# Performance work log

Hardware: AMD Instinct MI355X
Metric: run time of the kernel (lower is better)

## Reference

```python
import jax, jax.numpy as jnp
import numpy as np

N = 50000   # nodes
E = 800000  # edges (avg degree 16)
D = 128     # hidden_channels
L = 4       # num_layers
ALPHA = 0.1


def setup_inputs() -> dict:
    key = jax.random.key(0)
    ks = jax.random.split(key, 6)
    x = jax.random.normal(ks[0], (N, D), dtype=jnp.float32)
    w = jax.random.uniform(ks[1], (E,), dtype=jnp.float32)
    src = jax.random.randint(ks[2], (E,), 0, N)
    dst = jax.random.randint(ks[3], (E,), 0, N)
    # stacked per-layer Linear params
    W = jax.random.normal(ks[4], (L, D, D), dtype=jnp.float32) / np.float32(np.sqrt(D))
    b = jax.random.normal(ks[5], (L, D), dtype=jnp.float32) * 0.01
    # GPR coefficients: alpha*(1-alpha)^k, last = (1-alpha)^L
    temp_np = ALPHA * (1 - ALPHA) ** np.arange(L + 1)
    temp_np[-1] = (1 - ALPHA) ** L
    temp = jnp.asarray(temp_np, dtype=jnp.float32)
    return {"x": x, "w": w, "src": src, "dst": dst, "W": W, "b": b, "temp": temp}


def reference(x, w, src, dst, W, b, temp):
    # eval mode: dropout / dropout_adj are no-ops; edge_attn=False
    hidden = x * temp[0]
    for i in range(L):
        h = x @ W[i] + b[i]                 # [N, D] linear
        msg = h[src] * w[:, None]           # gather + edge-weight, [E, D]
        x = jax.ops.segment_sum(msg, dst, num_segments=N)  # scatter-sum
        x = jax.nn.relu(x)
        hidden = hidden + x * temp[i + 1]
    return hidden
```

## Files before the change

kernel.cpp:

```cpp
#include <hip/hip_runtime.h>
#include <hip/hip_fp16.h>

#define N_NODES 50000
#define N_EDGES 800000
#define DIM 128
#define LAYERS 4
#define SLOT 48
#define EPB 8

typedef __attribute__((ext_vector_type(8))) _Float16 half8;
typedef __attribute__((ext_vector_type(4))) float float4v;

__device__ __forceinline__ int pack_edge(int s, float w) {
    return (int)(((unsigned)__half_as_ushort(__float2half(w)) << 16) | (unsigned)(s & 0xFFFF));
}

__global__ __launch_bounds__(256) void init_kernel(const float4* __restrict__ x,
                                                   __half* __restrict__ xh, int n4) {
    int i = blockIdx.x * 256 + threadIdx.x;
    if (i >= n4) return;
    float4 v = x[i];
    union { __half2 hh[2]; float2 f2; } u;
    u.hh[0] = __floats2half2_rn(v.x, v.y);
    u.hh[1] = __floats2half2_rn(v.z, v.w);
    *(float2*)(xh + (size_t)i * 4) = u.f2;
}

__global__ __launch_bounds__(256) void bucket_kernel(const int* __restrict__ src,
                                                     const int* __restrict__ dst,
                                                     const float* __restrict__ w,
                                                     int* __restrict__ cnt,
                                                     int* __restrict__ edge_buf) {
    int g     = blockIdx.x & 7;
    int chunk = blockIdx.x >> 3;
    int base  = (chunk * 256 + threadIdx.x) * EPB;
    #pragma unroll
    for (int j = 0; j < EPB; j += 4) {
        int e = base + j;
        if (e >= N_EDGES) break;
        int4 d4 = *(const int4*)(dst + e);
        if ((d4.x & 7) == g) {
            int pos = atomicAdd(&cnt[d4.x], 1);
            edge_buf[(size_t)d4.x * SLOT + pos] = pack_edge(src[e + 0], w[e + 0]);
        }
        if ((d4.y & 7) == g) {
            int pos = atomicAdd(&cnt[d4.y], 1);
            edge_buf[(size_t)d4.y * SLOT + pos] = pack_edge(src[e + 1], w[e + 1]);
        }
        if ((d4.z & 7) == g) {
            int pos = atomicAdd(&cnt[d4.z], 1);
            edge_buf[(size_t)d4.z * SLOT + pos] = pack_edge(src[e + 2], w[e + 2]);
        }
        if ((d4.w & 7) == g) {
            int pos = atomicAdd(&cnt[d4.w], 1);
            edge_buf[(size_t)d4.w * SLOT + pos] = pack_edge(src[e + 3], w[e + 3]);
        }
    }
}

__global__ __launch_bounds__(256) void wt_prep_kernel(const float* __restrict__ W,
                                                      __half* __restrict__ Wt) {
    int i = blockIdx.x * 256 + threadIdx.x;
    if (i >= LAYERS * DIM * DIM) return;
    int l   = i >> 14;
    int rem = i & 16383;
    int k = rem >> 7;
    int n = rem & 127;
    Wt[(size_t)l * DIM * DIM + n * DIM + k] = __float2half(W[(size_t)l * DIM * DIM + k * DIM + n]);
}

__device__ __forceinline__ void batch8(const half8* __restrict__ h8,
                                       int m, int base, int cnt_r, int r, int c,
                                       float* accf, float& wsum) {
    half8 v[8]; float wv[8];
    #pragma unroll
    for (int u = 0; u < 8; ++u) {
        int jj = base + u;
        int p  = __shfl(m, (r << 4) | (jj & 15), 64);
        bool live = (jj < cnt_r);
        wv[u] = live
                  ? __half2float(__ushort_as_half((unsigned short)((unsigned)p >> 16)))
                  : 0.f;
        half8 vv = (half8)(0.f);
        if (live) vv = h8[(size_t)(p & 0xFFFF) * 16 + c];
        v[u] = vv;
    }
    #pragma unroll
    for (int u = 0; u < 8; ++u) {
        wsum += wv[u];
        #pragma unroll
        for (int t = 0; t < 8; ++t)
            accf[t] += wv[u] * (float)v[u][t];
    }
}

#define AP 136
template <bool FINAL>
__global__ __launch_bounds__(256) void layer_kernel(const half8* __restrict__ xin8,
                                                    const int* __restrict__ cnt_arr,
                                                    const int* __restrict__ edge_buf,
                                                    const __half* __restrict__ Wt,
                                                    const float* __restrict__ bl,
                                                    __half* __restrict__ xout_h,
                                                    float* __restrict__ hidden,
                                                    const float* __restrict__ temp,
                                                    const float* __restrict__ xf,
                                                    const half8* __restrict__ x1h,
                                                    const half8* __restrict__ x2h) {
    __shared__ __half Ah[16][AP];
    __shared__ float winS[16];
    int tid  = threadIdx.x;
    int wave = tid >> 6;
    int lane = tid & 63;
    int r = lane >> 4;
    int c = lane & 15;
    int node0  = blockIdx.x * 16 + wave * 4;
    int node_r = node0 + r;

    size_t mb = (size_t)node_r * SLOT;
    int m0 = edge_buf[mb + c];
    int m1 = edge_buf[mb + 16 + c];
    int m2 = edge_buf[mb + 32 + c];
    int4 c4 = *(const int4*)(cnt_arr + node0);

    int cnt_r = (r == 0) ? c4.x : (r == 1) ? c4.y : (r == 2) ? c4.z : c4.w;
    int maxc  = max(max(c4.x, c4.y), max(c4.z, c4.w));

    float accf[8];
    #pragma unroll
    for (int t = 0; t < 8; ++t) accf[t] = 0.f;
    float wsum = 0.f;

    batch8(xin8, m0, 0, cnt_r, r, c, accf, wsum);
    batch8(xin8, m0, 8, cnt_r, r, c, accf, wsum);
    if (maxc > 16) {
        batch8(xin8, m1, 16, cnt_r, r, c, accf, wsum);
        batch8(xin8, m1, 24, cnt_r, r, c, accf, wsum);
    }
    if (maxc > 32) {
        batch8(xin8, m2, 32, cnt_r, r, c, accf, wsum);
        batch8(xin8, m2, 40, cnt_r, r, c, accf, wsum);
    }

    union { __half2 hh[4]; float4 f4; } ua;
    ua.hh[0] = __floats2half2_rn(accf[0], accf[1]);
    ua.hh[1] = __floats2half2_rn(accf[2], accf[3]);
    ua.hh[2] = __floats2half2_rn(accf[4], accf[5]);
    ua.hh[3] = __floats2half2_rn(accf[6], accf[7]);
    int lr = wave * 4 + r;
    *(float4*)&Ah[lr][c * 8] = ua.f4;
    if (c == 0) winS[lr] = wsum;
    __syncthreads();

    int am  = lane & 15;
    int ak8 = (lane >> 4) * 8;
    float4v acc0 = (float4v)(0.f), acc1 = (float4v)(0.f);
    #pragma unroll
    for (int kk = 0; kk < 4; ++kk) {
        int k0 = kk * 32 + ak8;
        half8 a  = *(const half8*)&Ah[am][k0];
        half8 b0 = *(const half8*)(Wt + (size_t)(wave * 32 + am) * DIM + k0);
        half8 b1 = *(const half8*)(Wt + (size_t)(wave * 32 + 16 + am) * DIM + k0);
        acc0 = __builtin_amdgcn_mfma_f32_16x16x32_f16(a, b0, acc0, 0, 0, 0);
        acc1 = __builtin_amdgcn_mfma_f32_16x16x32_f16(a, b1, acc1, 0, 0, 0);
    }
    __syncthreads();

    int q  = lane >> 4;
    int cc = lane & 15;
    {
        int col = wave * 32 + cc;
        float bv = bl[col];
        #pragma unroll
        for (int j = 0; j < 4; ++j) {
            int row = q * 4 + j;
            Ah[row][col] = __float2half(fmaxf(acc0[j] + winS[row] * bv, 0.f));
        }
        col = wave * 32 + 16 + cc;
        bv = bl[col];
        #pragma unroll
        for (int j = 0; j < 4; ++j) {
            int row = q * 4 + j;
            Ah[row][col] = __float2half(fmaxf(acc1[j] + winS[row] * bv, 0.f));
        }
    }
    __syncthreads();

    int row = tid >> 4;
    int ch  = tid & 15;
    int gnode = blockIdx.x * 16 + row;
    size_t o = (size_t)gnode * DIM + ch * 8;
    half8 hv = *(const half8*)&Ah[row][ch * 8];

    if constexpr (!FINAL) {
        *(float4*)(xout_h + o) = *(float4*)&hv;
    } else {
        float t0 = temp[0], t1 = temp[1], t2 = temp[2], t3 = temp[3], t4 = temp[4];
        size_t ro = (size_t)gnode * 16 + ch;
        half8 v1 = x1h[ro];
        half8 v2 = x2h[ro];
        half8 v3 = xin8[ro];
        float4 x0a = *(const float4*)(xf + o);
        float4 x0b = *(const float4*)(xf + o + 4);
        float out[8];
        out[0] = t0 * x0a.x; out[1] = t0 * x0a.y; out[2] = t0 * x0a.z; out[3] = t0 * x0a.w;
        out[4] = t0 * x0b.x; out[5] = t0 * x0b.y; out[6] = t0 * x0b.z; out[7] = t0 * x0b.w;
        #pragma unroll
        for (int t = 0; t < 8; ++t)
            out[t] += t1 * (float)v1[t] + t2 * (float)v2[t]
                    + t3 * (float)v3[t] + t4 * (float)hv[t];
        float4 h0 = make_float4(out[0], out[1], out[2], out[3]);
        float4 h1 = make_float4(out[4], out[5], out[6], out[7]);
        *(float4*)(hidden + o)     = h0;
        *(float4*)(hidden + o + 4) = h1;
    }
}

extern "C" void kernel_launch(void* const* d_in, const int* in_sizes, int n_in,
                              void* d_out, int out_size, void* d_ws, size_t ws_size,
                              hipStream_t stream) {
    const float* x    = (const float*)d_in[0];
    const float* w    = (const float*)d_in[1];
    const int*   src  = (const int*)d_in[2];
    const int*   dst  = (const int*)d_in[3];
    const float* W    = (const float*)d_in[4];
    const float* b    = (const float*)d_in[5];
    const float* temp = (const float*)d_in[6];
    float* hidden = (float*)d_out;

    char* ws = (char*)d_ws;
    __half* xhA      = (__half*)ws;                   ws += (size_t)N_NODES * DIM * sizeof(__half);
    __half* xhB      = (__half*)ws;                   ws += (size_t)N_NODES * DIM * sizeof(__half);
    __half* xhC      = (__half*)ws;                   ws += (size_t)N_NODES * DIM * sizeof(__half);
    __half* Wt       = (__half*)ws;                   ws += (size_t)LAYERS * DIM * DIM * sizeof(__half);
    int*    cnt      = (int*)ws;                      ws += (size_t)N_NODES * sizeof(int);
    int*    edge_buf = (int*)ws;                      ws += (size_t)(N_NODES * SLOT + 64) * sizeof(int);

    const int n4 = N_NODES * DIM / 4;

    hipMemsetAsync(cnt, 0, (size_t)N_NODES * sizeof(int), stream);
    {
        int chunks = (N_EDGES + 256 * EPB - 1) / (256 * EPB);
        bucket_kernel<<<chunks * 8, 256, 0, stream>>>(src, dst, w, cnt, edge_buf);
    }
    wt_prep_kernel<<<(LAYERS * DIM * DIM + 255) / 256, 256, 0, stream>>>(W, Wt);

    init_kernel<<<(n4 + 255) / 256, 256, 0, stream>>>((const float4*)x, xhA, n4);

    const int layer_blocks = N_NODES / 16;
    layer_kernel<false><<<layer_blocks, 256, 0, stream>>>(
        (const half8*)xhA, cnt, edge_buf, Wt + 0 * DIM * DIM, b + 0 * DIM,
        xhB, hidden, temp, x, nullptr, nullptr);
    layer_kernel<false><<<layer_blocks, 256, 0, stream>>>(
        (const half8*)xhB, cnt, edge_buf, Wt + 1 * DIM * DIM, b + 1 * DIM,
        xhC, hidden, temp, x, nullptr, nullptr);
    layer_kernel<false><<<layer_blocks, 256, 0, stream>>>(
        (const half8*)xhC, cnt, edge_buf, Wt + 2 * DIM * DIM, b + 2 * DIM,
        xhA, hidden, temp, x, nullptr, nullptr);
    layer_kernel<true><<<layer_blocks, 256, 0, stream>>>(
        (const half8*)xhA, cnt, edge_buf, Wt + 3 * DIM * DIM, b + 3 * DIM,
        nullptr, hidden, temp, x, (const half8*)xhB, (const half8*)xhC);
}
```

Baseline: 287.2 us.

## Fuse bucket, weight-prep and init kernels into one prep launch

Merges the edge bucketing, weight transpose/convert and input fp16 conversion kernels into a single kernel that dispatches on block index, removing two launches and letting the independent work overlap. The bucketing path now loads src and w with vector loads instead of scalar loads. The layer kernel gets a minimum-occupancy launch bound of 6 and loads the third edge slot only when a node has more than 32 edges. The occupancy hint may force register spilling.

```diff
diff --git a/kernel.cpp b/kernel.cpp
--- a/kernel.cpp
+++ b/kernel.cpp
@@ -8,6 +8,10 @@
 #define SLOT 48
 #define EPB 8
 
+#define BUCKET_BLOCKS 3128
+#define WT_BLOCKS 256
+#define INIT_BLOCKS 6250
+
 typedef __attribute__((ext_vector_type(8))) _Float16 half8;
 typedef __attribute__((ext_vector_type(4))) float float4v;
 
@@ -15,58 +19,61 @@
     return (int)(((unsigned)__half_as_ushort(__float2half(w)) << 16) | (unsigned)(s & 0xFFFF));
 }
 
-__global__ __launch_bounds__(256) void init_kernel(const float4* __restrict__ x,
-                                                   __half* __restrict__ xh, int n4) {
-    int i = blockIdx.x * 256 + threadIdx.x;
-    if (i >= n4) return;
-    float4 v = x[i];
-    union { __half2 hh[2]; float2 f2; } u;
-    u.hh[0] = __floats2half2_rn(v.x, v.y);
-    u.hh[1] = __floats2half2_rn(v.z, v.w);
-    *(float2*)(xh + (size_t)i * 4) = u.f2;
-}
-
-__global__ __launch_bounds__(256) void bucket_kernel(const int* __restrict__ src,
-                                                     const int* __restrict__ dst,
-                                                     const float* __restrict__ w,
-                                                     int* __restrict__ cnt,
-                                                     int* __restrict__ edge_buf) {
-    int g     = blockIdx.x & 7;
-    int chunk = blockIdx.x >> 3;
-    int base  = (chunk * 256 + threadIdx.x) * EPB;
-    #pragma unroll
-    for (int j = 0; j < EPB; j += 4) {
-        int e = base + j;
-        if (e >= N_EDGES) break;
-        int4 d4 = *(const int4*)(dst + e);
-        if ((d4.x & 7) == g) {
-            int pos = atomicAdd(&cnt[d4.x], 1);
-            edge_buf[(size_t)d4.x * SLOT + pos] = pack_edge(src[e + 0], w[e + 0]);
-        }
-        if ((d4.y & 7) == g) {
-            int pos = atomicAdd(&cnt[d4.y], 1);
-            edge_buf[(size_t)d4.y * SLOT + pos] = pack_edge(src[e + 1], w[e + 1]);
-        }
-        if ((d4.z & 7) == g) {
-            int pos = atomicAdd(&cnt[d4.z], 1);
-            edge_buf[(size_t)d4.z * SLOT + pos] = pack_edge(src[e + 2], w[e + 2]);
-        }
-        if ((d4.w & 7) == g) {
-            int pos = atomicAdd(&cnt[d4.w], 1);
-            edge_buf[(size_t)d4.w * SLOT + pos] = pack_edge(src[e + 3], w[e + 3]);
-        }
-    }
-}
-
-__global__ __launch_bounds__(256) void wt_prep_kernel(const float* __restrict__ W,
-                                                      __half* __restrict__ Wt) {
-    int i = blockIdx.x * 256 + threadIdx.x;
-    if (i >= LAYERS * DIM * DIM) return;
-    int l   = i >> 14;
-    int rem = i & 16383;
-    int k = rem >> 7;
-    int n = rem & 127;
-    Wt[(size_t)l * DIM * DIM + n * DIM + k] = __float2half(W[(size_t)l * DIM * DIM + k * DIM + n]);
+__device__ __forceinline__ void bucket_one(int d, int s, float wv, int g,
+                                           int* __restrict__ cnt,
+                                           int* __restrict__ edge_buf) {
+    if ((d & 7) == g) {
+        int pos = atomicAdd(&cnt[d], 1);
+        edge_buf[(size_t)d * SLOT + pos] = pack_edge(s, wv);
+    }
+}
+
+__global__ __launch_bounds__(256) void prep_kernel(const int* __restrict__ src,
+                                                   const int* __restrict__ dst,
+                                                   const float* __restrict__ w,
+                                                   int* __restrict__ cnt,
+                                                   int* __restrict__ edge_buf,
+                                                   const float* __restrict__ W,
+                                                   __half* __restrict__ Wt,
+                                                   const float4* __restrict__ x,
+                                                   __half* __restrict__ xh) {
+    int bid = blockIdx.x;
+    int tid = threadIdx.x;
+    if (bid < BUCKET_BLOCKS) {
+        int g     = bid & 7;
+        int chunk = bid >> 3;
+        int base  = (chunk * 256 + tid) * EPB;
+        if (base >= N_EDGES) return;
+        int4   d4a = *(const int4*)(dst + base);
+        int4   d4b = *(const int4*)(dst + base + 4);
+        int4   s4a = *(const int4*)(src + base);
+        int4   s4b = *(const int4*)(src + base + 4);
+        float4 w4a = *(const float4*)(w + base);
+        float4 w4b = *(const float4*)(w + base + 4);
+        bucket_one(d4a.x, s4a.x, w4a.x, g, cnt, edge_buf);
+        bucket_one(d4a.y, s4a.y, w4a.y, g, cnt, edge_buf);
+        bucket_one(d4a.z, s4a.z, w4a.z, g, cnt, edge_buf);
+        bucket_one(d4a.w, s4a.w, w4a.w, g, cnt, edge_buf);
+        bucket_one(d4b.x, s4b.x, w4b.x, g, cnt, edge_buf);
+        bucket_one(d4b.y, s4b.y, w4b.y, g, cnt, edge_buf);
+        bucket_one(d4b.z, s4b.z, w4b.z, g, cnt, edge_buf);
+        bucket_one(d4b.w, s4b.w, w4b.w, g, cnt, edge_buf);
+    } else if (bid < BUCKET_BLOCKS + WT_BLOCKS) {
+        int i = (bid - BUCKET_BLOCKS) * 256 + tid;
+        int l   = i >> 14;
+        int rem = i & 16383;
+        int k = rem >> 7;
+        int n = rem & 127;
+        Wt[(size_t)l * DIM * DIM + n * DIM + k] =
+            __float2half(W[(size_t)l * DIM * DIM + k * DIM + n]);
+    } else {
+        int i = (bid - BUCKET_BLOCKS - WT_BLOCKS) * 256 + tid;
+        float4 v = x[i];
+        union { __half2 hh[2]; float2 f2; } u;
+        u.hh[0] = __floats2half2_rn(v.x, v.y);
+        u.hh[1] = __floats2half2_rn(v.z, v.w);
+        *(float2*)(xh + (size_t)i * 4) = u.f2;
+    }
 }
 
 __device__ __forceinline__ void batch8(const half8* __restrict__ h8,
@@ -96,7 +103,7 @@
 
 #define AP 136
 template <bool FINAL>
-__global__ __launch_bounds__(256) void layer_kernel(const half8* __restrict__ xin8,
+__global__ __launch_bounds__(256, 6) void layer_kernel(const half8* __restrict__ xin8,
                                                     const int* __restrict__ cnt_arr,
                                                     const int* __restrict__ edge_buf,
                                                     const __half* __restrict__ Wt,
@@ -120,7 +127,6 @@
     size_t mb = (size_t)node_r * SLOT;
     int m0 = edge_buf[mb + c];
     int m1 = edge_buf[mb + 16 + c];
-    int m2 = edge_buf[mb + 32 + c];
     int4 c4 = *(const int4*)(cnt_arr + node0);
 
     int cnt_r = (r == 0) ? c4.x : (r == 1) ? c4.y : (r == 2) ? c4.z : c4.w;
@@ -138,6 +144,7 @@
         batch8(xin8, m1, 24, cnt_r, r, c, accf, wsum);
     }
     if (maxc > 32) {
+        int m2 = edge_buf[mb + 32 + c];
         batch8(xin8, m2, 32, cnt_r, r, c, accf, wsum);
         batch8(xin8, m2, 40, cnt_r, r, c, accf, wsum);
     }
@@ -236,16 +243,9 @@
     int*    cnt      = (int*)ws;                      ws += (size_t)N_NODES * sizeof(int);
     int*    edge_buf = (int*)ws;                      ws += (size_t)(N_NODES * SLOT + 64) * sizeof(int);
 
-    const int n4 = N_NODES * DIM / 4;
-
     hipMemsetAsync(cnt, 0, (size_t)N_NODES * sizeof(int), stream);
-    {
-        int chunks = (N_EDGES + 256 * EPB - 1) / (256 * EPB);
-        bucket_kernel<<<chunks * 8, 256, 0, stream>>>(src, dst, w, cnt, edge_buf);
-    }
-    wt_prep_kernel<<<(LAYERS * DIM * DIM + 255) / 256, 256, 0, stream>>>(W, Wt);
-
-    init_kernel<<<(n4 + 255) / 256, 256, 0, stream>>>((const float4*)x, xhA, n4);
+    prep_kernel<<<BUCKET_BLOCKS + WT_BLOCKS + INIT_BLOCKS, 256, 0, stream>>>(
+        src, dst, w, cnt, edge_buf, W, Wt, (const float4*)x, xhA);
 
     const int layer_blocks = N_NODES / 16;
     layer_kernel<false><<<layer_blocks, 256, 0, stream>>>(
```

After: 500.8 us. 74.4% more time.
